# Performance work log

Measured on AMD Instinct MI355X. Metric: run time of the kernel, lower is better.

## Reference

```python
import jax, jax.numpy as jnp
import numpy as np

V, E, DIN, DOUT, NREL2 = 80000, 640000, 128, 128, 500
EPS = 1e-5


def ccorr(a, b):
    # circular cross-correlation: irfft(conj(rfft(a)) * rfft(b))
    fa = jnp.fft.rfft(a, axis=-1)
    fb = jnp.fft.rfft(b, axis=-1)
    return jnp.fft.irfft(jnp.conj(fa) * fb, n=a.shape[-1], axis=-1)


def setup_inputs() -> dict:
    key = jax.random.key(0)
    ks = jax.random.split(key, 14)
    s = 0.1  # xavier-ish scale
    return {
        'x': jax.random.normal(ks[0], (V, DIN), jnp.float32),
        'x_t': jnp.zeros((V, 16), jnp.float32),
        'x_i': jnp.zeros((V, 16), jnp.float32),
        'x_n': jnp.zeros((V, 16), jnp.float32),
        'rel_repr': jax.random.normal(ks[1], (NREL2, DIN), jnp.float32) * s,
        'edge_norm': jax.random.uniform(ks[2], (E,), jnp.float32),
        'in_w': jax.random.normal(ks[3], (DIN, DOUT), jnp.float32) * s,
        'out_w': jax.random.normal(ks[4], (DIN, DOUT), jnp.float32) * s,
        'loop_w': jax.random.normal(ks[5], (DIN, DOUT), jnp.float32) * s,
        'w_rel': jax.random.normal(ks[6], (DIN, DOUT), jnp.float32) * s,
        'loop_rel': jax.random.normal(ks[7], (1, DIN), jnp.float32) * s,
        'attn_w': jax.random.normal(ks[8], (3 * DIN,), jnp.float32) * 0.05,
        'bias': jnp.zeros((DOUT,), jnp.float32),
        'src': jax.random.randint(ks[9], (E,), 0, V),
        'dst': jax.random.randint(ks[10], (E,), 0, V),
        'edge_type': jax.random.randint(ks[11], (E,), 0, NREL2),
    }


def reference(x, x_t, x_i, x_n, rel_repr, edge_norm, in_w, out_w, loop_w,
              w_rel, loop_rel, attn_w, bias, src, dst, edge_type):
    nV = x.shape[0]
    nE = src.shape[0]
    rel = rel_repr  # rel_wt is None (num_base <= 0)

    src_h = x[src]              # [E, din] gather
    dst_h = x[dst]              # [E, din]
    rel_h = rel[edge_type]      # [E, din]

    # edge attention: attn_fc(cat[src,rel,dst]) == split-weight form
    w_s, w_r, w_d = jnp.split(attn_w, 3)
    e = jax.nn.leaky_relu(src_h @ w_s + rel_h @ w_r + dst_h @ w_d, 0.01)  # [E]

    # message: FFT composition then half in_w / half out_w
    edh = ccorr(src_h, rel_h)                                  # [E, din]
    half = nE // 2
    msg = jnp.concatenate([edh[:half] @ in_w, edh[half:] @ out_w], axis=0)
    msg = jax.nn.softmax(msg, axis=1)  # F.softmax default dim=1 for 2D
    msg = msg * edge_norm[:, None]

    # segment softmax of e over destination-node mailboxes
    emax = jax.ops.segment_max(e, dst, num_segments=nV)
    emax = jnp.where(jnp.isfinite(emax), emax, 0.0)
    ee = jnp.exp(e - emax[dst])
    esum = jax.ops.segment_sum(ee, dst, num_segments=nV)
    alpha = ee / jnp.where(esum[dst] > 0, esum[dst], 1.0)      # [E]

    h = jax.ops.segment_sum(alpha[:, None] * msg, dst, num_segments=nV) / 3.0

    # self-loop branch
    loop = ccorr(x, jnp.broadcast_to(loop_rel, x.shape)) @ loop_w / 3.0

    out = h + loop + bias
    # BatchNorm1d, training mode, affine weight=1 bias=0 (default init)
    mean = out.mean(axis=0)
    var = out.var(axis=0)
    out = (out - mean) / jnp.sqrt(var + EPS)
    return out, rel @ w_rel
```

## Files before the change

kernel.cpp:

```cpp
#include <hip/hip_runtime.h>

#define V 80000
#define E 640000
#define D 128
#define NREL 500
#define HALF (E/2)
#define NGROUP 1000
#define EP (E + NGROUP * 32)
#define NBLK_D ((V + 1023) / 1024)
#define NREP 320
#define SLABLOG 11
#define SLAB 2048
#define NSLAB ((E + SLAB - 1) / SLAB)

typedef __attribute__((ext_vector_type(8))) short s8v;
typedef __attribute__((ext_vector_type(4))) float f4v;
typedef __attribute__((ext_vector_type(4))) int i4v;
typedef unsigned long long u64;

__device__ __forceinline__ unsigned short f2bf(float f) {
  unsigned u = __float_as_uint(f);
  return (unsigned short)((u + 0x7fffu + ((u >> 16) & 1u)) >> 16);
}

__global__ void k_init(u64* packed, int* hist, uint4* edat) {
  int i = blockIdx.x * 256 + threadIdx.x;
  if (i < V) packed[i] = 0ull;
  if (i < NGROUP * NREP) hist[i] = 0;
  if (i < EP) { uint4 r; r.x = 0; r.y = 0xFFFFFFFFu; r.z = 0; r.w = 0; edat[i] = r; }
}

__global__ void k_prep(const float* __restrict__ rel, const float* __restrict__ w_rel,
                       const float* __restrict__ attn_w, const float* __restrict__ loop_rel,
                       const float* __restrict__ loop_w, const float* __restrict__ in_w,
                       const float* __restrict__ out_w, float* __restrict__ out1,
                       float* __restrict__ rw, unsigned short* __restrict__ relb,
                       unsigned short* __restrict__ mltb, unsigned short* __restrict__ wtb) {
  int b = blockIdx.x, n = threadIdx.x;
  if (b < NREL) {
    __shared__ float rs[D];
    __shared__ float red[D];
    float rv = rel[b * D + n];
    rs[n] = rv;
    relb[b * D + n] = f2bf(rv);
    red[n] = rv * attn_w[D + n];
    __syncthreads();
    float acc = 0.f;
    #pragma unroll 8
    for (int j = 0; j < D; ++j) acc += rs[j] * w_rel[j * D + n];
    out1[b * D + n] = acc;
    if (n == 0) {
      float s = 0.f;
      for (int j = 0; j < D; ++j) s += red[j];
      rw[b] = s;
    }
  } else if (b < NREL + D) {
    int j = b - NREL;
    __shared__ float ls[2 * D];
    ls[n] = loop_rel[n]; ls[n + D] = loop_rel[n];
    __syncthreads();
    float acc = 0.f;
    #pragma unroll 8
    for (int k = 0; k < D; ++k) acc += ls[j + k] * loop_w[k * D + n];
    mltb[n * D + j] = f2bf(acc);
  } else {
    int bw = b - NREL - D;
    int h = bw >> 7, n2 = bw & 127;
    const float* W = h ? out_w : in_w;
    wtb[h * 16384 + n2 * D + n] = f2bf(W[n * D + n2]);
  }
}

__global__ void k_xbproj(const float* __restrict__ x, const float* __restrict__ attn_w,
                         unsigned* __restrict__ xb32, float* __restrict__ sxw,
                         float* __restrict__ dxw) {
  int tid = threadIdx.x;
  int wid = tid >> 6, lane = tid & 63;
  float ws0 = attn_w[2 * lane], ws1 = attn_w[2 * lane + 1];
  float wd0 = attn_w[256 + 2 * lane], wd1 = attn_w[256 + 2 * lane + 1];
  for (int v = blockIdx.x * 4 + wid; v < V; v += 2048 * 4) {
    float2 xv = *(const float2*)&x[(size_t)v * D + 2 * lane];
    float ps = xv.x * ws0 + xv.y * ws1;
    float pd = xv.x * wd0 + xv.y * wd1;
    #pragma unroll
    for (int off = 32; off; off >>= 1) { ps += __shfl_xor(ps, off); pd += __shfl_xor(pd, off); }
    if (lane == 0) { sxw[v] = ps; dxw[v] = pd; }
    xb32[(size_t)v * 64 + lane] = (unsigned)f2bf(xv.x) | ((unsigned)f2bf(xv.y) << 16);
  }
}

__global__ __launch_bounds__(256) void k_mbt2(const unsigned short* __restrict__ relb,
    const unsigned short* __restrict__ wtb, unsigned short* __restrict__ mbt) {
  __shared__ unsigned short relp[256];
  __shared__ unsigned short Wl[D * D];
  int g = blockIdx.x, tid = threadIdx.x;
  int t = (g >= NREL) ? g - NREL : g;
  const unsigned short* wt = wtb + (g >= NREL ? 16384 : 0);
  relp[tid] = relb[t * D + (tid & 127)];
  #pragma unroll
  for (int i = 0; i < 8; ++i) {
    int idx = tid + i * 256;
    int n = idx >> 4, kc = idx & 15;
    *(uint4*)((char*)Wl + n * 256 + ((kc ^ (n & 7)) << 4)) = *(const uint4*)(wt + n * D + kc * 8);
  }
  __syncthreads();
  int wid = tid >> 6, ln = tid & 15, hi = (tid & 63) >> 4;
  s8v af[2][4];
  #pragma unroll
  for (int m = 0; m < 2; ++m) {
    int j = wid * 32 + m * 16 + ln;
    #pragma unroll
    for (int ks = 0; ks < 4; ++ks) {
      int o = j + ks * 32 + hi * 8;
      s8v a;
      #pragma unroll
      for (int i = 0; i < 8; ++i) a[i] = (short)relp[o + i];
      af[m][ks] = a;
    }
  }
  f4v acc[2][8];
  #pragma unroll
  for (int m = 0; m < 2; ++m)
    #pragma unroll
    for (int nn = 0; nn < 8; ++nn) acc[m][nn] = (f4v){0.f, 0.f, 0.f, 0.f};
  #pragma unroll
  for (int ks = 0; ks < 4; ++ks) {
    #pragma unroll
    for (int nn = 0; nn < 8; ++nn) {
      int n2 = nn * 16 + ln;
      int kc = (ks * 4 + hi) ^ (n2 & 7);
      s8v b = *(const s8v*)((const char*)Wl + n2 * 256 + (kc << 4));
      #pragma unroll
      for (int m = 0; m < 2; ++m)
        acc[m][nn] = __builtin_amdgcn_mfma_f32_16x16x32_bf16(af[m][ks], b, acc[m][nn], 0, 0, 0);
    }
  }
  size_t gb = (size_t)g * (D * D);
  #pragma unroll
  for (int m = 0; m < 2; ++m)
    #pragma unroll
    for (int nn = 0; nn < 8; ++nn) {
      int jb = wid * 32 + m * 16 + hi * 4;
      u64 pk = (u64)f2bf(acc[m][nn][0])
        | ((u64)f2bf(acc[m][nn][1]) << 16)
        | ((u64)f2bf(acc[m][nn][2]) << 32)
        | ((u64)f2bf(acc[m][nn][3]) << 48);
      *(u64*)&mbt[gb + (size_t)(nn * 16 + ln) * D + jb] = pk;
    }
}

__global__ __launch_bounds__(256) void k_lgemm(const unsigned short* __restrict__ xb,
    const unsigned short* __restrict__ mltb, const float* __restrict__ bias,
    float* __restrict__ out0) {
  __shared__ unsigned short Wl[D * D];
  int tid = threadIdx.x;
  #pragma unroll
  for (int i = 0; i < 8; ++i) {
    int idx = tid + i * 256;
    int n = idx >> 4, kc = idx & 15;
    *(uint4*)((char*)Wl + n * 256 + ((kc ^ (n & 7)) << 4)) = *(const uint4*)(mltb + n * D + kc * 8);
  }
  __syncthreads();
  int wid = tid >> 6, ln = tid & 15, hi = (tid & 63) >> 4;
  int rbase = blockIdx.x * 128 + wid * 32;
  s8v af[2][4];
  #pragma unroll
  for (int m = 0; m < 2; ++m)
    #pragma unroll
    for (int ks = 0; ks < 4; ++ks)
      af[m][ks] = *(const s8v*)(xb + (size_t)(rbase + m * 16 + ln) * D + ks * 32 + hi * 8);
  f4v acc[2][8];
  #pragma unroll
  for (int m = 0; m < 2; ++m)
    #pragma unroll
    for (int nn = 0; nn < 8; ++nn) acc[m][nn] = (f4v){0.f, 0.f, 0.f, 0.f};
  #pragma unroll
  for (int ks = 0; ks < 4; ++ks) {
    #pragma unroll
    for (int nn = 0; nn < 8; ++nn) {
      int n2 = nn * 16 + ln;
      int kc = (ks * 4 + hi) ^ (n2 & 7);
      s8v b = *(const s8v*)((const char*)Wl + n2 * 256 + (kc << 4));
      #pragma unroll
      for (int m = 0; m < 2; ++m)
        acc[m][nn] = __builtin_amdgcn_mfma_f32_16x16x32_bf16(af[m][ks], b, acc[m][nn], 0, 0, 0);
    }
  }
  float bcol[8];
  #pragma unroll
  for (int nn = 0; nn < 8; ++nn) bcol[nn] = bias[nn * 16 + ln];
  #pragma unroll
  for (int m = 0; m < 2; ++m)
    #pragma unroll
    for (int nn = 0; nn < 8; ++nn)
      #pragma unroll
      for (int r = 0; r < 4; ++r)
        out0[(size_t)(rbase + m * 16 + hi * 4 + r) * D + nn * 16 + ln] =
            acc[m][nn][r] * (1.f / 3.f) + bcol[nn];
}

__global__ __launch_bounds__(512) void k_edge(const int* __restrict__ src,
                       const int* __restrict__ dst,
                       const int* __restrict__ et, const float* __restrict__ sxw,
                       const float* __restrict__ dxw, const float* __restrict__ rw,
                       float* __restrict__ evals, u64* __restrict__ packed,
                       int* __restrict__ hist, unsigned short* __restrict__ drank,
                       unsigned short* __restrict__ grank) {
  __shared__ int lhist[NGROUP];
  int r = blockIdx.x, tid = threadIdx.x;
  for (int t = tid; t < NGROUP; t += 512) lhist[t] = 0;
  __syncthreads();
  #pragma unroll
  for (int c = 0; c < 4; ++c) {
    int i = r * SLAB + c * 512 + tid;
    if (i < E) {
      int d = dst[i];
      float ev = sxw[src[i]] + rw[et[i]] + dxw[d];
      ev = ev >= 0.f ? ev : 0.01f * ev;
      float xv = __expf(ev);
      evals[i] = xv;
      u64 inc = (1ull << 48) + (u64)(xv * 65536.f + 0.5f);
      u64 old = atomicAdd(&packed[d], inc);
      drank[i] = (unsigned short)(old >> 48);
      int g = et[i] + ((i >= HALF) ? NREL : 0);
      int gr = atomicAdd(&lhist[g], 1);
      grank[i] = (unsigned short)gr;
    }
  }
  __syncthreads();
  for (int t = tid; t < NGROUP; t += 512) hist[t * NREP + r] = lhist[t];
}

__global__ void k_gmeta(const int* __restrict__ hist, int* __restrict__ cnt,
                        int* __restrict__ rowpref) {
  int wv = (blockIdx.x * 256 + threadIdx.x) >> 6;
  int lane = threadIdx.x & 63;
  if (wv >= NGROUP) return;
  int running = 0;
  #pragma unroll
  for (int c = 0; c < NREP / 64; ++c) {
    int r = c * 64 + lane;
    int v = hist[wv * NREP + r];
    int inc = v;
    #pragma unroll
    for (int off = 1; off < 64; off <<= 1) {
      int u = __shfl_up(inc, off);
      if (lane >= off) inc += u;
    }
    rowpref[wv * NREP + r] = running + inc - v;
    running += __shfl(inc, 63);
  }
  if (lane == 63) cnt[wv] = running;
}

__global__ void k_scan(const int* __restrict__ cnt, int* __restrict__ poffs) {
  __shared__ int tmp[1024];
  int t = threadIdx.x;
  int c = (t < NGROUP) ? cnt[t] : 0;
  int pc = (c + 31) & ~31;
  tmp[t] = pc;
  __syncthreads();
  #pragma unroll
  for (int off = 1; off < 1024; off <<= 1) {
    int v = (t >= off) ? tmp[t - off] : 0;
    __syncthreads();
    tmp[t] += v;
    __syncthreads();
  }
  poffs[t] = tmp[t] - pc;
}

__global__ void k_dscan1(const u64* __restrict__ packed, float* __restrict__ esum,
                         int* __restrict__ dloc, int* __restrict__ dtot) {
  __shared__ int tmp[1024];
  int t = threadIdx.x;
  int i = blockIdx.x * 1024 + t;
  int v = 0;
  if (i < V) {
    u64 q = packed[i];
    esum[i] = (float)(q & 0xFFFFFFFFFFFFull) * (1.f / 65536.f);
    v = (int)(q >> 48);
  }
  tmp[t] = v;
  __syncthreads();
  #pragma unroll
  for (int off = 1; off < 1024; off <<= 1) {
    int u = (t >= off) ? tmp[t - off] : 0;
    __syncthreads();
    tmp[t] += u;
    __syncthreads();
  }
  if (i < V) dloc[i] = tmp[t] - v;
  if (t == 1023) dtot[blockIdx.x] = tmp[t];
}

__global__ void k_dscan3(const int* __restrict__ dloc, const int* __restrict__ dtot,
                         int* __restrict__ doffs) {
  __shared__ int sh[128];
  int t = threadIdx.x;
  if (t < 128) sh[t] = (t < NBLK_D) ? dtot[t] : 0;
  __syncthreads();
  #pragma unroll
  for (int off = 1; off < 128; off <<= 1) {
    int v = (t >= off && t < 128) ? sh[t - off] : 0;
    __syncthreads();
    if (t < 128) sh[t] += v;
    __syncthreads();
  }
  int bo = (blockIdx.x == 0) ? 0 : sh[blockIdx.x - 1];
  int i = blockIdx.x * 1024 + t;
  if (i < V) doffs[i] = dloc[i] + bo;
  if (i == 0) doffs[V] = E;
}

__global__ void k_scatter(const int* __restrict__ src, const int* __restrict__ dst,
                          const int* __restrict__ et, const float* __restrict__ ee,
                          const float* __restrict__ esum, const float* __restrict__ enorm,
                          const int* __restrict__ poffs, const int* __restrict__ rowpref,
                          const int* __restrict__ doffs,
                          const unsigned short* __restrict__ drank,
                          const unsigned short* __restrict__ grank,
                          uint4* __restrict__ edat) {
  int i = blockIdx.x * 256 + threadIdx.x;
  if (i >= E) return;
  int g = et[i] + ((i >= HALF) ? NREL : 0);
  int r = i >> SLABLOG;
  int pos = poffs[g] + rowpref[g * NREP + r] + (int)grank[i];
  int d = dst[i];
  uint4 rec;
  rec.x = (unsigned)src[i];
  rec.y = (unsigned)(doffs[d] + (int)drank[i]);
  rec.z = __float_as_uint(ee[i] / esum[d] * enorm[i] * (1.f / 3.f));
  rec.w = 0;
  edat[pos] = rec;
}

__global__ __launch_bounds__(256) void k_msg3(const unsigned short* __restrict__ xb,
    const unsigned short* __restrict__ mbt, const int* __restrict__ cnt,
    const int* __restrict__ poffs, const uint4* __restrict__ edat,
    const int* __restrict__ doffs, int loNode, int hiNode,
    unsigned short* __restrict__ msgb) {
  __shared__ uint4 Blds4[(D * 272) / 16];
  unsigned char* Bldsb = (unsigned char*)Blds4;
  int g = blockIdx.x;
  int c = cnt[g];
  if (c == 0) return;
  int tid = threadIdx.x;
  const uint4* Mg = (const uint4*)(mbt + (size_t)g * (D * D));
  #pragma unroll
  for (int i = 0; i < 8; ++i) {
    int idx = tid + i * 256;
    int row = idx >> 4, col = (idx & 15) * 16;
    Blds4[(row * 272 + col) >> 4] = Mg[idx];
  }
  __syncthreads();
  int b1 = doffs[loNode];
  int b2 = doffs[hiNode];
  int wid = tid >> 6, ln = tid & 15, hi = (tid & 63) >> 4;
  int base0 = poffs[g];
  int nch = (c + 15) >> 4;
  int ch = wid;
  uint4 recp;
  s8v afp[4];
  if (ch < nch) {
    recp = edat[base0 + ch * 16 + ln];
    const unsigned short* xr = xb + (size_t)recp.x * D + hi * 8;
    #pragma unroll
    for (int ks = 0; ks < 4; ++ks) afp[ks] = *(const s8v*)(xr + ks * 32);
  }
  for (; ch < nch; ch += 4) {
    uint4 recc = recp;
    int nc2 = ch + 4;
    if (nc2 < nch) recp = edat[base0 + nc2 * 16 + ln];
    s8v afc[4];
    #pragma unroll
    for (int ks = 0; ks < 4; ++ks) afc[ks] = afp[ks];
    f4v acc[8];
    #pragma unroll
    for (int n = 0; n < 8; ++n) acc[n] = (f4v){0.f, 0.f, 0.f, 0.f};
    #pragma unroll
    for (int ks = 0; ks < 4; ++ks) {
      #pragma unroll
      for (int n = 0; n < 8; ++n) {
        int row = n * 16 + ln;
        s8v bf = *(const s8v*)(Bldsb + row * 272 + ks * 64 + hi * 16);
        acc[n] = __builtin_amdgcn_mfma_f32_16x16x32_bf16(afc[ks], bf, acc[n], 0, 0, 0);
      }
    }
    if (nc2 < nch) {
      const unsigned short* xr = xb + (size_t)recp.x * D + hi * 8;
      #pragma unroll
      for (int ks = 0; ks < 4; ++ks) afp[ks] = *(const s8v*)(xr + ks * 32);
    }
    f4v sum = (f4v){0.f, 0.f, 0.f, 0.f};
    #pragma unroll
    for (int n = 0; n < 8; ++n)
      #pragma unroll
      for (int j = 0; j < 4; ++j) {
        float e = __expf(acc[n][j]);
        acc[n][j] = e;
        sum[j] += e;
      }
    #pragma unroll
    for (int off = 1; off < 16; off <<= 1)
      #pragma unroll
      for (int j = 0; j < 4; ++j) sum[j] += __shfl_xor(sum[j], off);
    #pragma unroll
    for (int j = 0; j < 4; ++j) {
      int dpos = __shfl((int)recc.y, hi * 4 + j, 16);
      if (dpos >= b1 && dpos < b2) {
        float cf = __uint_as_float(__shfl((int)recc.z, hi * 4 + j, 16));
        size_t rowb = (size_t)(dpos - b1) * D;
        float s = cf / sum[j];
        unsigned q0 = (unsigned)f2bf(acc[0][j] * s) | ((unsigned)f2bf(acc[1][j] * s) << 16);
        unsigned q1 = (unsigned)f2bf(acc[2][j] * s) | ((unsigned)f2bf(acc[3][j] * s) << 16);
        unsigned q2 = (unsigned)f2bf(acc[4][j] * s) | ((unsigned)f2bf(acc[5][j] * s) << 16);
        unsigned q3 = (unsigned)f2bf(acc[6][j] * s) | ((unsigned)f2bf(acc[7][j] * s) << 16);
        uint4 qv; qv.x = q0; qv.y = q1; qv.z = q2; qv.w = q3;
        *(uint4*)&msgb[rowb + ln * 8] = qv;
      }
    }
  }
}

__global__ void k_sum(const unsigned short* __restrict__ msgb, const int* __restrict__ doffs,
                      float* __restrict__ out0, int loNode, int hiNode) {
  int tid = threadIdx.x;
  int wid = tid >> 6, lane = tid & 63;
  int sub = lane >> 4, ln = lane & 15;
  int d = loNode + blockIdx.x * 16 + wid * 4 + sub;
  if (d >= hiNode) return;
  int b1 = doffs[loNode];
  int s0 = doffs[d];
  int len = doffs[d + 1] - s0;
  const unsigned short* mp = msgb + (size_t)(s0 - b1) * D + ln * 8;
  float a[8];
  #pragma unroll
  for (int n = 0; n < 8; ++n) a[n] = 0.f;
  for (int r = 0; r < len; ++r) {
    uint4 q = *(const uint4*)(mp + (size_t)r * D);
    a[0] += __uint_as_float(q.x << 16);
    a[1] += __uint_as_float(q.x & 0xffff0000u);
    a[2] += __uint_as_float(q.y << 16);
    a[3] += __uint_as_float(q.y & 0xffff0000u);
    a[4] += __uint_as_float(q.z << 16);
    a[5] += __uint_as_float(q.z & 0xffff0000u);
    a[6] += __uint_as_float(q.w << 16);
    a[7] += __uint_as_float(q.w & 0xffff0000u);
  }
  float* orow = out0 + (size_t)d * D + ln;
  #pragma unroll
  for (int n = 0; n < 8; ++n) orow[n * 16] += a[n];
}

__global__ void k_bn1(const float* __restrict__ out0, float* __restrict__ part) {
  __shared__ float sh[256];
  int tid = threadIdx.x;
  int col = tid & 127, r = tid >> 7;
  float s = 0.f, q = 0.f;
  for (int v = blockIdx.x * 2 + r; v < V; v += 1024) {
    float val = out0[(size_t)v * D + col];
    s += val; q += val * val;
  }
  sh[tid] = s;
  __syncthreads();
  if (r == 0) part[blockIdx.x * 256 + col] = sh[col] + sh[col + 128];
  __syncthreads();
  sh[tid] = q;
  __syncthreads();
  if (r == 0) part[blockIdx.x * 256 + 128 + col] = sh[col] + sh[col + 128];
}

__global__ void k_bn2(const float* __restrict__ part, float* __restrict__ mrs) {
  __shared__ float sh[256];
  int t = threadIdx.x;
  float s = 0.f;
  for (int b = 0; b < 512; ++b) s += part[b * 256 + t];
  sh[t] = s;
  __syncthreads();
  if (t < 128) {
    float mean = sh[t] * (1.f / V);
    float var = sh[128 + t] * (1.f / V) - mean * mean;
    mrs[t] = mean;
    mrs[128 + t] = rsqrtf(var + 1e-5f);
  }
}

__global__ void k_bn_norm(float* __restrict__ out0, const float* __restrict__ mrs) {
  int i = blockIdx.x * 256 + threadIdx.x;
  if (i >= V * D) return;
  int c = i & 127;
  out0[i] = (out0[i] - mrs[c]) * mrs[128 + c];
}

extern "C" void kernel_launch(void* const* d_in, const int* in_sizes, int n_in,
                              void* d_out, int out_size, void* d_ws, size_t ws_size,
                              hipStream_t stream) {
  const float* x        = (const float*)d_in[0];
  const float* rel      = (const float*)d_in[4];
  const float* enorm    = (const float*)d_in[5];
  const float* in_w     = (const float*)d_in[6];
  const float* out_w    = (const float*)d_in[7];
  const float* loop_w   = (const float*)d_in[8];
  const float* w_rel    = (const float*)d_in[9];
  const float* loop_rel = (const float*)d_in[10];
  const float* attn_w   = (const float*)d_in[11];
  const float* bias     = (const float*)d_in[12];
  const int* src = (const int*)d_in[13];
  const int* dst = (const int*)d_in[14];
  const int* et  = (const int*)d_in[15];

  float* out0 = (float*)d_out;
  float* out1 = out0 + (size_t)V * D;

  float* base = (float*)d_ws;
  size_t off = 0;
  float* sxw = base + off;      off += V;
  float* dxw = base + off;      off += V;
  float* esum = base + off;     off += V;
  float* evals = base + off;    off += E;
  float* rw = base + off;       off += 512;
  float* part = base + off;     off += 512 * 256;
  float* mrs = base + off;      off += 256;
  int* cnt = (int*)(base + off);   off += 1024;
  int* poffs = (int*)(base + off); off += 1024;
  int* hist = (int*)(base + off);     off += NGROUP * NREP;
  int* rowpref = (int*)(base + off);  off += NGROUP * NREP;
  u64* packed = (u64*)(base + off);   off += 2 * V;
  int* dloc = (int*)(base + off);  off += V;
  int* doffs = (int*)(base + off); off += V + 2;
  int* dtot = (int*)(base + off);  off += 128;
  unsigned short* drank = (unsigned short*)(base + off); off += E / 2;
  unsigned short* grank = (unsigned short*)(base + off); off += E / 2;
  uint4* edat = (uint4*)(base + off); off += (size_t)4 * EP;
  unsigned short* mltb = (unsigned short*)(base + off); off += D * D / 2;
  unsigned short* relb = (unsigned short*)(base + off); off += NREL * D / 2;
  unsigned short* wtb  = (unsigned short*)(base + off); off += 2 * D * D / 2;
  unsigned short* xb   = (unsigned short*)(base + off); off += (size_t)V * D / 2;
  unsigned short* mbt  = (unsigned short*)(base + off); off += (size_t)NGROUP * D * D / 2;
  unsigned short* msgb = (unsigned short*)(base + off);

  size_t availF = (ws_size / 4 > off) ? (ws_size / 4 - off) : 0;
  int ns = 1;
  if ((size_t)EP * (D / 2) > availF) {
    ns = 2;
    while (ns < 64 && (size_t)(E / ns + 16384) * (D / 2) > availF) ns *= 2;
  }

  k_init<<<(EP + 255) / 256, 256, 0, stream>>>(packed, hist, edat);
  k_prep<<<NREL + D + 256, 128, 0, stream>>>(rel, w_rel, attn_w, loop_rel, loop_w,
                                             in_w, out_w, out1, rw, relb, mltb, wtb);
  k_xbproj<<<2048, 256, 0, stream>>>(x, attn_w, (unsigned*)xb, sxw, dxw);
  k_mbt2<<<NGROUP, 256, 0, stream>>>(relb, wtb, mbt);
  k_lgemm<<<V / 128, 256, 0, stream>>>(xb, mltb, bias, out0);
  k_edge<<<NSLAB, 512, 0, stream>>>(src, dst, et, sxw, dxw, rw,
                                    evals, packed, hist, drank, grank);
  k_gmeta<<<(NGROUP * 64 + 255) / 256, 256, 0, stream>>>(hist, cnt, rowpref);
  k_scan<<<1, 1024, 0, stream>>>(cnt, poffs);
  k_dscan1<<<NBLK_D, 1024, 0, stream>>>(packed, esum, dloc, dtot);
  k_dscan3<<<NBLK_D, 1024, 0, stream>>>(dloc, dtot, doffs);
  k_scatter<<<(E + 255) / 256, 256, 0, stream>>>(src, dst, et, evals, esum, enorm,
                                                 poffs, rowpref, doffs, drank, grank, edat);
  int Vs = V / ns;
  for (int s = 0; s < ns; ++s) {
    int lo = s * Vs, hi = (s == ns - 1) ? V : (s + 1) * Vs;
    k_msg3<<<NGROUP, 256, 0, stream>>>(xb, mbt, cnt, poffs, edat,
                                       doffs, lo, hi, msgb);
    k_sum<<<(Vs + 15) / 16, 256, 0, stream>>>(msgb, doffs, out0, lo, hi);
  }
  k_bn1<<<512, 256, 0, stream>>>(out0, part);
  k_bn2<<<1, 256, 0, stream>>>(part, mrs);
  k_bn_norm<<<(V * D + 255) / 256, 256, 0, stream>>>(out0, mrs);
}
```

Baseline: 325.9 us.

## Fuse BatchNorm statistics into segment-sum kernel and vectorize x bf16 projection

The per-column sum and sum-of-squares for BatchNorm are now computed inside k_sum right after each output row is updated. Per-block partials go to a larger partial buffer, which a two-stage reduction (k_bn2a, k_bn2b) folds into the mean and inverse std, removing the separate full pass over the 80000x128 output. k_xbproj now loads 8 floats per lane and writes uint4 bf16 packs. The message-packing step in k_msg3 uses the hardware v_cvt_pk_bf16_f32 instruction instead of manual rounding. The extra shuffles and LDS work in k_sum add some cost, and the partial buffer assumes at most MAXPART blocks in total.

```diff
diff --git a/kernel.cpp b/kernel.cpp
--- a/kernel.cpp
+++ b/kernel.cpp
@@ -12,6 +12,7 @@
 #define SLABLOG 11
 #define SLAB 2048
 #define NSLAB ((E + SLAB - 1) / SLAB)
+#define MAXPART 5008
 
 typedef __attribute__((ext_vector_type(8))) short s8v;
 typedef __attribute__((ext_vector_type(4))) float f4v;
@@ -21,6 +22,11 @@
 __device__ __forceinline__ unsigned short f2bf(float f) {
   unsigned u = __float_as_uint(f);
   return (unsigned short)((u + 0x7fffu + ((u >> 16) & 1u)) >> 16);
+}
+__device__ __forceinline__ unsigned cvtpk(float lo, float hi) {
+  unsigned r;
+  asm("v_cvt_pk_bf16_f32 %0, %1, %2" : "=v"(r) : "v"(lo), "v"(hi));
+  return r;
 }
 
 __global__ void k_init(u64* packed, int* hist, uint4* edat) {
@@ -72,20 +78,38 @@
 }
 
 __global__ void k_xbproj(const float* __restrict__ x, const float* __restrict__ attn_w,
-                         unsigned* __restrict__ xb32, float* __restrict__ sxw,
+                         uint4* __restrict__ xb4, float* __restrict__ sxw,
                          float* __restrict__ dxw) {
   int tid = threadIdx.x;
   int wid = tid >> 6, lane = tid & 63;
-  float ws0 = attn_w[2 * lane], ws1 = attn_w[2 * lane + 1];
-  float wd0 = attn_w[256 + 2 * lane], wd1 = attn_w[256 + 2 * lane + 1];
-  for (int v = blockIdx.x * 4 + wid; v < V; v += 2048 * 4) {
-    float2 xv = *(const float2*)&x[(size_t)v * D + 2 * lane];
-    float ps = xv.x * ws0 + xv.y * ws1;
-    float pd = xv.x * wd0 + xv.y * wd1;
-    #pragma unroll
-    for (int off = 32; off; off >>= 1) { ps += __shfl_xor(ps, off); pd += __shfl_xor(pd, off); }
-    if (lane == 0) { sxw[v] = ps; dxw[v] = pd; }
-    xb32[(size_t)v * 64 + lane] = (unsigned)f2bf(xv.x) | ((unsigned)f2bf(xv.y) << 16);
+  int sub = lane >> 4, ln = lane & 15;
+  float ws[8], wd[8];
+  #pragma unroll
+  for (int i = 0; i < 8; ++i) {
+    ws[i] = attn_w[ln * 8 + i];
+    wd[i] = attn_w[256 + ln * 8 + i];
+  }
+  for (int v = blockIdx.x * 16 + wid * 4 + sub; v < V; v += 2048 * 16) {
+    f4v x0 = *(const f4v*)&x[(size_t)v * D + ln * 8];
+    f4v x1 = *(const f4v*)&x[(size_t)v * D + ln * 8 + 4];
+    float ps = 0.f, pd = 0.f;
+    #pragma unroll
+    for (int i = 0; i < 4; ++i) {
+      ps += x0[i] * ws[i] + x1[i] * ws[4 + i];
+      pd += x0[i] * wd[i] + x1[i] * wd[4 + i];
+    }
+    #pragma unroll
+    for (int off = 1; off < 16; off <<= 1) {
+      ps += __shfl_xor(ps, off);
+      pd += __shfl_xor(pd, off);
+    }
+    if (ln == 0) { sxw[v] = ps; dxw[v] = pd; }
+    uint4 qv;
+    qv.x = (unsigned)f2bf(x0[0]) | ((unsigned)f2bf(x0[1]) << 16);
+    qv.y = (unsigned)f2bf(x0[2]) | ((unsigned)f2bf(x0[3]) << 16);
+    qv.z = (unsigned)f2bf(x1[0]) | ((unsigned)f2bf(x1[1]) << 16);
+    qv.w = (unsigned)f2bf(x1[2]) | ((unsigned)f2bf(x1[3]) << 16);
+    xb4[(size_t)v * 16 + ln] = qv;
   }
 }
 
@@ -412,11 +436,11 @@
         float cf = __uint_as_float(__shfl((int)recc.z, hi * 4 + j, 16));
         size_t rowb = (size_t)(dpos - b1) * D;
         float s = cf / sum[j];
-        unsigned q0 = (unsigned)f2bf(acc[0][j] * s) | ((unsigned)f2bf(acc[1][j] * s) << 16);
-        unsigned q1 = (unsigned)f2bf(acc[2][j] * s) | ((unsigned)f2bf(acc[3][j] * s) << 16);
-        unsigned q2 = (unsigned)f2bf(acc[4][j] * s) | ((unsigned)f2bf(acc[5][j] * s) << 16);
-        unsigned q3 = (unsigned)f2bf(acc[6][j] * s) | ((unsigned)f2bf(acc[7][j] * s) << 16);
-        uint4 qv; qv.x = q0; qv.y = q1; qv.z = q2; qv.w = q3;
+        uint4 qv;
+        qv.x = cvtpk(acc[0][j] * s, acc[1][j] * s);
+        qv.y = cvtpk(acc[2][j] * s, acc[3][j] * s);
+        qv.z = cvtpk(acc[4][j] * s, acc[5][j] * s);
+        qv.w = cvtpk(acc[6][j] * s, acc[7][j] * s);
         *(uint4*)&msgb[rowb + ln * 8] = qv;
       }
     }
@@ -424,58 +448,85 @@
 }
 
 __global__ void k_sum(const unsigned short* __restrict__ msgb, const int* __restrict__ doffs,
-                      float* __restrict__ out0, int loNode, int hiNode) {
+                      float* __restrict__ out0, float* __restrict__ part,
+                      int loNode, int hiNode, int partBase) {
+  __shared__ float shs[4][128];
+  __shared__ float shq[4][128];
   int tid = threadIdx.x;
   int wid = tid >> 6, lane = tid & 63;
   int sub = lane >> 4, ln = lane & 15;
   int d = loNode + blockIdx.x * 16 + wid * 4 + sub;
-  if (d >= hiNode) return;
-  int b1 = doffs[loNode];
-  int s0 = doffs[d];
-  int len = doffs[d + 1] - s0;
-  const unsigned short* mp = msgb + (size_t)(s0 - b1) * D + ln * 8;
-  float a[8];
-  #pragma unroll
-  for (int n = 0; n < 8; ++n) a[n] = 0.f;
-  for (int r = 0; r < len; ++r) {
-    uint4 q = *(const uint4*)(mp + (size_t)r * D);
-    a[0] += __uint_as_float(q.x << 16);
-    a[1] += __uint_as_float(q.x & 0xffff0000u);
-    a[2] += __uint_as_float(q.y << 16);
-    a[3] += __uint_as_float(q.y & 0xffff0000u);
-    a[4] += __uint_as_float(q.z << 16);
-    a[5] += __uint_as_float(q.z & 0xffff0000u);
-    a[6] += __uint_as_float(q.w << 16);
-    a[7] += __uint_as_float(q.w & 0xffff0000u);
-  }
-  float* orow = out0 + (size_t)d * D + ln;
-  #pragma unroll
-  for (int n = 0; n < 8; ++n) orow[n * 16] += a[n];
-}
-
-__global__ void k_bn1(const float* __restrict__ out0, float* __restrict__ part) {
-  __shared__ float sh[256];
-  int tid = threadIdx.x;
-  int col = tid & 127, r = tid >> 7;
-  float s = 0.f, q = 0.f;
-  for (int v = blockIdx.x * 2 + r; v < V; v += 1024) {
-    float val = out0[(size_t)v * D + col];
-    s += val; q += val * val;
-  }
-  sh[tid] = s;
-  __syncthreads();
-  if (r == 0) part[blockIdx.x * 256 + col] = sh[col] + sh[col + 128];
-  __syncthreads();
-  sh[tid] = q;
-  __syncthreads();
-  if (r == 0) part[blockIdx.x * 256 + 128 + col] = sh[col] + sh[col + 128];
-}
-
-__global__ void k_bn2(const float* __restrict__ part, float* __restrict__ mrs) {
+  float v[8];
+  #pragma unroll
+  for (int n = 0; n < 8; ++n) v[n] = 0.f;
+  if (d < hiNode) {
+    int b1 = doffs[loNode];
+    int s0 = doffs[d];
+    int len = doffs[d + 1] - s0;
+    const unsigned short* mp = msgb + (size_t)(s0 - b1) * D + ln * 8;
+    float a[8];
+    #pragma unroll
+    for (int n = 0; n < 8; ++n) a[n] = 0.f;
+    for (int r = 0; r < len; ++r) {
+      uint4 q = *(const uint4*)(mp + (size_t)r * D);
+      a[0] += __uint_as_float(q.x << 16);
+      a[1] += __uint_as_float(q.x & 0xffff0000u);
+      a[2] += __uint_as_float(q.y << 16);
+      a[3] += __uint_as_float(q.y & 0xffff0000u);
+      a[4] += __uint_as_float(q.z << 16);
+      a[5] += __uint_as_float(q.z & 0xffff0000u);
+      a[6] += __uint_as_float(q.w << 16);
+      a[7] += __uint_as_float(q.w & 0xffff0000u);
+    }
+    float* orow = out0 + (size_t)d * D + ln;
+    #pragma unroll
+    for (int n = 0; n < 8; ++n) {
+      float t = orow[n * 16] + a[n];
+      orow[n * 16] = t;
+      v[n] = t;
+    }
+  }
+  float s[8], q2[8];
+  #pragma unroll
+  for (int n = 0; n < 8; ++n) { s[n] = v[n]; q2[n] = v[n] * v[n]; }
+  #pragma unroll
+  for (int off = 16; off < 64; off <<= 1)
+    #pragma unroll
+    for (int n = 0; n < 8; ++n) {
+      s[n] += __shfl_xor(s[n], off);
+      q2[n] += __shfl_xor(q2[n], off);
+    }
+  if (sub == 0) {
+    #pragma unroll
+    for (int n = 0; n < 8; ++n) {
+      shs[wid][n * 16 + ln] = s[n];
+      shq[wid][n * 16 + ln] = q2[n];
+    }
+  }
+  __syncthreads();
+  if (wid == 0) {
+    float* pb = part + (size_t)(partBase + blockIdx.x) * 256;
+    for (int c = lane; c < 128; c += 64) {
+      pb[c] = shs[0][c] + shs[1][c] + shs[2][c] + shs[3][c];
+      pb[128 + c] = shq[0][c] + shq[1][c] + shq[2][c] + shq[3][c];
+    }
+  }
+}
+
+__global__ void k_bn2a(const float* __restrict__ part, float* __restrict__ part2,
+                       int rows, int rpb) {
+  int t = threadIdx.x, b = blockIdx.x;
+  int r1 = (b + 1) * rpb; if (r1 > rows) r1 = rows;
+  float s = 0.f;
+  for (int r = b * rpb; r < r1; ++r) s += part[(size_t)r * 256 + t];
+  part2[b * 256 + t] = s;
+}
+
+__global__ void k_bn2b(const float* __restrict__ part2, float* __restrict__ mrs) {
   __shared__ float sh[256];
   int t = threadIdx.x;
   float s = 0.f;
-  for (int b = 0; b < 512; ++b) s += part[b * 256 + t];
+  for (int b = 0; b < 100; ++b) s += part2[b * 256 + t];
   sh[t] = s;
   __syncthreads();
   if (t < 128) {
@@ -520,7 +571,8 @@
   float* esum = base + off;     off += V;
   float* evals = base + off;    off += E;
   float* rw = base + off;       off += 512;
-  float* part = base + off;     off += 512 * 256;
+  float* part = base + off;     off += (size_t)MAXPART * 256;
+  float* part2 = base + off;    off += 100 * 256;
   float* mrs = base + off;      off += 256;
   int* cnt = (int*)(base + off);   off += 1024;
   int* poffs = (int*)(base + off); off += 1024;
@@ -550,7 +602,7 @@
   k_init<<<(EP + 255) / 256, 256, 0, stream>>>(packed, hist, edat);
   k_prep<<<NREL + D + 256, 128, 0, stream>>>(rel, w_rel, attn_w, loop_rel, loop_w,
                                              in_w, out_w, out1, rw, relb, mltb, wtb);
-  k_xbproj<<<2048, 256, 0, stream>>>(x, attn_w, (unsigned*)xb, sxw, dxw);
+  k_xbproj<<<2048, 256, 0, stream>>>(x, attn_w, (uint4*)xb, sxw, dxw);
   k_mbt2<<<NGROUP, 256, 0, stream>>>(relb, wtb, mbt);
   k_lgemm<<<V / 128, 256, 0, stream>>>(xb, mltb, bias, out0);
   k_edge<<<NSLAB, 512, 0, stream>>>(src, dst, et, sxw, dxw, rw,
@@ -562,13 +614,17 @@
   k_scatter<<<(E + 255) / 256, 256, 0, stream>>>(src, dst, et, evals, esum, enorm,
                                                  poffs, rowpref, doffs, drank, grank, edat);
   int Vs = V / ns;
+  int partBase = 0;
   for (int s = 0; s < ns; ++s) {
     int lo = s * Vs, hi = (s == ns - 1) ? V : (s + 1) * Vs;
+    int nb = (hi - lo + 15) / 16;
     k_msg3<<<NGROUP, 256, 0, stream>>>(xb, mbt, cnt, poffs, edat,
                                        doffs, lo, hi, msgb);
-    k_sum<<<(Vs + 15) / 16, 256, 0, stream>>>(msgb, doffs, out0, lo, hi);
-  }
-  k_bn1<<<512, 256, 0, stream>>>(out0, part);
-  k_bn2<<<1, 256, 0, stream>>>(part, mrs);
+    k_sum<<<nb, 256, 0, stream>>>(msgb, doffs, out0, part, lo, hi, partBase);
+    partBase += nb;
+  }
+  int rpb = (partBase + 99) / 100;
+  k_bn2a<<<100, 256, 0, stream>>>(part, part2, partBase, rpb);
+  k_bn2b<<<1, 256, 0, stream>>>(part2, mrs);
   k_bn_norm<<<(V * D + 255) / 256, 256, 0, stream>>>(out0, mrs);
 }
```

Result: faster. 308.1 us (-5.5%).
